# Optimization experiments

Measured on AMD Instinct MI355X. Metric: run time of the kernel, lower is better.

The kernel has to match this reference:

```python
import jax, jax.numpy as jnp
import numpy as np

IN_F = 128
OUT_F = 64
HEAD = 4
ALPHA = 0.1
N, S = 32, 1024
OH = OUT_F * HEAD


def setup_inputs() -> dict:
    key = jax.random.key(0)
    k_h, k_adj, k_W, k_a = jax.random.split(key, 4)
    h = jax.random.normal(k_h, (N, S, IN_F), dtype=jnp.float32)
    adj = jax.random.uniform(k_adj, (N, S, S), dtype=jnp.float32)
    # xavier_uniform with gain=1.414
    gain = 1.414
    lim_W = gain * np.sqrt(6.0 / (IN_F + OH))
    W = jax.random.uniform(k_W, (IN_F, OH), dtype=jnp.float32, minval=-lim_W, maxval=lim_W)
    lim_a = gain * np.sqrt(6.0 / (2 * OH + 1))
    a = jax.random.uniform(k_a, (2 * OH, 1), dtype=jnp.float32, minval=-lim_a, maxval=lim_a)
    return {"h": h, "adj": adj, "W": W, "a": a}


def reference(h, adj, W, a):
    # h: (N, S, F_in); adj unused in original forward
    Wh = jnp.einsum('nsf,fo->nso', h, W)  # (N, S, OH)
    a1 = a[:OH, 0]   # source half of concat weight
    a2 = a[OH:, 0]   # target half
    # concat([Wh_i, Wh_j]) @ a == Wh_i@a1 + Wh_j@a2  (avoids (N,S,S,2*OH) tensor)
    f = Wh @ a1  # (N, S)
    g = Wh @ a2  # (N, S)
    e = f[:, :, None] + g[:, None, :]          # (N, S, S)
    e = jnp.where(e > 0, e, ALPHA * e)          # LeakyReLU
    attention = jax.nn.softmax(e, axis=2)
    out = jnp.einsum('nij,njo->nio', attention, Wh)  # (N, S, OH)
    # split into HEAD chunks of OUT_F, stack, mean over heads
    out = out.reshape(N, S, HEAD, OUT_F).mean(axis=2)
    # ELU
    return jnp.where(out > 0, out, jnp.expm1(out))
```

## Files before the change

### kernel.cpp

```cpp
#include <hip/hip_runtime.h>
#include <math.h>

#define SQ    1024
#define INF   128
#define OUTF  64
#define OHH   256
#define LOG2E 1.44269504088896f

using bf16x8 = __attribute__((ext_vector_type(8))) __bf16;
using bf16x4 = __attribute__((ext_vector_type(4))) __bf16;
using f32x4  = __attribute__((ext_vector_type(4))) float;
using u16x8  = __attribute__((ext_vector_type(8))) unsigned short;

#if __has_builtin(__builtin_amdgcn_exp2f)
#define EXP2F(x) __builtin_amdgcn_exp2f(x)
#else
#define EXP2F(x) __expf((x) * 0.6931471805599453f)
#endif

__global__ __launch_bounds__(256) void kA(
    const float* __restrict__ h, const float* __restrict__ W,
    const float* __restrict__ a, __bf16* __restrict__ whmH,
    __bf16* __restrict__ whmL, float* __restrict__ fo, float* __restrict__ go)
{
    __shared__ __bf16 wmfH[8192];
    __shared__ __bf16 wmfL[8192];
    __shared__ float  wfl[INF], wgl[INF];
    __shared__ float  al[2 * OHH];

    const int t    = threadIdx.x;
    const int lane = t & 63;
    const int w    = t >> 6;
    const int R0   = blockIdx.x * 64;

    al[t]       = a[t];
    al[t + 256] = a[t + 256];

    for (int g = t; g < 2048; g += 256) {
        const int k  = g >> 4;
        const int n0 = (g & 15) << 2;
        const float* Wp = W + k * OHH + n0;
        float4 w0 = *(const float4*)Wp;
        float4 w1 = *(const float4*)(Wp + 64);
        float4 w2 = *(const float4*)(Wp + 128);
        float4 w3 = *(const float4*)(Wp + 192);
        float wm4[4] = {0.25f * (w0.x + w1.x + w2.x + w3.x),
                        0.25f * (w0.y + w1.y + w2.y + w3.y),
                        0.25f * (w0.z + w1.z + w2.z + w3.z),
                        0.25f * (w0.w + w1.w + w2.w + w3.w)};
        const int c = k >> 5, kq = (k >> 3) & 3, id8 = k & 7, T = n0 >> 4;
        const int lbase = kq * 16 + (n0 & 15);
        #pragma unroll
        for (int j = 0; j < 4; ++j) {
            float  v  = wm4[j];
            __bf16 hb = (__bf16)v;
            const int o = ((c * 4 + T) * 64 + lbase + j) * 8 + id8;
            wmfH[o] = hb;
            wmfL[o] = (__bf16)(v - (float)hb);
        }
    }
    __syncthreads();

    {
        const int row = t & 127;
        const float4* Wr = (const float4*)(W + row * OHH);
        const float4* av = (const float4*)(t < 128 ? al : al + OHH);
        float s = 0.f;
        for (int q = 0; q < OHH / 4; ++q) {
            float4 wv = Wr[q], x = av[q];
            s += wv.x * x.x + wv.y * x.y + wv.z * x.z + wv.w * x.w;
        }
        if (t < 128) wfl[row] = s * LOG2E;
        else         wgl[row] = s * LOG2E;
    }
    __syncthreads();

    const int m  = lane & 15;
    const int kq = lane >> 4;
    const float* hrow = h + (size_t)(R0 + w * 16 + m) * INF + kq * 8;

    f32x4 acc[4] = {};
    float sf = 0.f, sg = 0.f;

    #pragma unroll
    for (int c = 0; c < 4; ++c) {
        float4 v0 = *(const float4*)(hrow + c * 32);
        float4 v1 = *(const float4*)(hrow + c * 32 + 4);
        float hv[8] = {v0.x, v0.y, v0.z, v0.w, v1.x, v1.y, v1.z, v1.w};

        float4 wf0 = *(const float4*)(wfl + c * 32 + kq * 8);
        float4 wf1 = *(const float4*)(wfl + c * 32 + kq * 8 + 4);
        float4 wg0 = *(const float4*)(wgl + c * 32 + kq * 8);
        float4 wg1 = *(const float4*)(wgl + c * 32 + kq * 8 + 4);
        float wfv[8] = {wf0.x, wf0.y, wf0.z, wf0.w, wf1.x, wf1.y, wf1.z, wf1.w};
        float wgv[8] = {wg0.x, wg0.y, wg0.z, wg0.w, wg1.x, wg1.y, wg1.z, wg1.w};

        u16x8  ahu;
        bf16x8 alo;
        #pragma unroll
        for (int i = 0; i < 8; ++i) {
            float v = hv[i];
            sf = fmaf(v, wfv[i], sf);
            sg = fmaf(v, wgv[i], sg);
            unsigned u = __float_as_uint(v);
            ahu[i] = (unsigned short)(u >> 16);
            alo[i] = (__bf16)(v - __uint_as_float(u & 0xFFFF0000u));
        }
        bf16x8 ah = __builtin_bit_cast(bf16x8, ahu);

        #pragma unroll
        for (int T = 0; T < 4; ++T) {
            bf16x8 bh = *(const bf16x8*)&wmfH[((c * 4 + T) * 64 + lane) * 8];
            bf16x8 bl = *(const bf16x8*)&wmfL[((c * 4 + T) * 64 + lane) * 8];
            acc[T] = __builtin_amdgcn_mfma_f32_16x16x32_bf16(ah,  bh, acc[T], 0, 0, 0);
            acc[T] = __builtin_amdgcn_mfma_f32_16x16x32_bf16(alo, bh, acc[T], 0, 0, 0);
            acc[T] = __builtin_amdgcn_mfma_f32_16x16x32_bf16(ah,  bl, acc[T], 0, 0, 0);
        }
    }

    sf += __shfl_xor(sf, 16, 64); sf += __shfl_xor(sf, 32, 64);
    sg += __shfl_xor(sg, 16, 64); sg += __shfl_xor(sg, 32, 64);
    if (lane < 16) {
        fo[R0 + w * 16 + m] = sf;
        go[R0 + w * 16 + m] = sg;
    }

    {
        const int n     = R0 >> 10;
        const int Jb    = ((R0 & 1023) >> 5) + (w >> 1);
        const int jj3   = 2 * (w & 1) + (kq >> 1);
        const int laneS = jj3 * 16 + m;
        const int idx0  = (kq & 1) * 4;
        #pragma unroll
        for (int T = 0; T < 4; ++T) {
            const size_t base =
                (((size_t)(n * 32 + Jb) * 4 + T) * 64 + laneS) * 8 + idx0;
            bf16x4 hv, lv;
            #pragma unroll
            for (int r = 0; r < 4; ++r) {
                float  v  = acc[T][r];
                __bf16 hb = (__bf16)v;
                hv[r] = hb;
                lv[r] = (__bf16)(v - (float)hb);
            }
            *(bf16x4*)(whmH + base) = hv;
            *(bf16x4*)(whmL + base) = lv;
        }
    }
}

__global__ __launch_bounds__(256) void kC(
    const __bf16* __restrict__ whmH, const __bf16* __restrict__ whmL,
    const float* __restrict__ fi, const float* __restrict__ gi,
    float* __restrict__ out)
{
    __shared__ float  gl[SQ];
    __shared__ float  fl[64];
    __shared__ __bf16 bfr[3][4096];

    const int t     = threadIdx.x;
    const int lane  = t & 63;
    const int wid   = t >> 6;
    const int n     = blockIdx.x & 31;
    const int itile = blockIdx.x >> 5;
    const int i0    = itile * 64;

    const char* gHb = (const char*)(whmH + (size_t)n * 65536) + wid * 1024 + lane * 16;
    const char* gLb = (const char*)(whmL + (size_t)n * 65536) + wid * 1024 + lane * 16;

    auto stage = [&](int J, int buf) {
        char* lH = (char*)&bfr[buf][0] + wid * 1024;
        char* lL = (char*)&bfr[buf][2048] + wid * 1024;
        __builtin_amdgcn_global_load_lds(
            (const __attribute__((address_space(1))) unsigned int*)(gHb + (size_t)J * 4096),
            (__attribute__((address_space(3))) unsigned int*)lH, 16, 0, 0);
        __builtin_amdgcn_global_load_lds(
            (const __attribute__((address_space(1))) unsigned int*)(gLb + (size_t)J * 4096),
            (__attribute__((address_space(3))) unsigned int*)lL, 16, 0, 0);
    };

    ((float4*)gl)[t] = ((const float4*)(gi + n * SQ))[t];
    if (t < 64) fl[t] = fi[n * SQ + i0 + t];

    stage(0, 0);
    stage(1, 1);
    __syncthreads();

    const float myf = fl[wid * 16 + (lane & 15)];
    const int   kq  = lane >> 4;

    f32x4 acc[4] = {};
    float lsum = 0.f;

    for (int J = 0; J < 32; ++J) {
        float4 g0 = *(const float4*)&gl[J * 32 + kq * 8];
        float4 g1 = *(const float4*)&gl[J * 32 + kq * 8 + 4];
        float gs8[8] = {g0.x, g0.y, g0.z, g0.w, g1.x, g1.y, g1.z, g1.w};

        u16x8  phu;
        bf16x8 pl;
        #pragma unroll
        for (int idx = 0; idx < 8; ++idx) {
            float e  = myf + gs8[idx];
            float lr = fmaxf(e, 0.1f * e);
            float p  = EXP2F(lr);
            lsum += p;
            unsigned u = __float_as_uint(p);
            phu[idx] = (unsigned short)(u >> 16);
            pl[idx]  = (__bf16)(p - __uint_as_float(u & 0xFFFF0000u));
        }
        bf16x8 ph = __builtin_bit_cast(bf16x8, phu);

        __syncthreads();
        if (J + 2 < 32) stage(J + 2, (J + 2) % 3);

        const bf16x8* fr = (const bf16x8*)&bfr[J % 3][0];
        #pragma unroll
        for (int T = 0; T < 4; ++T) {
            bf16x8 bh = fr[T * 64 + lane];
            bf16x8 bl = fr[(4 + T) * 64 + lane];
            acc[T] = __builtin_amdgcn_mfma_f32_16x16x32_bf16(ph, bh, acc[T], 0, 0, 0);
            acc[T] = __builtin_amdgcn_mfma_f32_16x16x32_bf16(pl, bh, acc[T], 0, 0, 0);
            acc[T] = __builtin_amdgcn_mfma_f32_16x16x32_bf16(ph, bl, acc[T], 0, 0, 0);
        }
    }

    lsum += __shfl_xor(lsum, 16, 64);
    lsum += __shfl_xor(lsum, 32, 64);
    const float rv = 1.0f / lsum;

    const int rq = lane >> 4;
    float scs[4];
    #pragma unroll
    for (int r = 0; r < 4; ++r)
        scs[r] = __shfl(rv, rq * 4 + r, 64);

    const int colbase = lane & 15;
    #pragma unroll
    for (int T = 0; T < 4; ++T) {
        #pragma unroll
        for (int r = 0; r < 4; ++r) {
            int   rr = rq * 4 + r;
            float v  = acc[T][r] * scs[r];
            v = v > 0.f ? v : expm1f(v);
            out[(size_t)(n * SQ + i0 + wid * 16 + rr) * OUTF + T * 16 + colbase] = v;
        }
    }
}

extern "C" void kernel_launch(void* const* d_in, const int* in_sizes, int n_in,
                              void* d_out, int out_size, void* d_ws, size_t ws_size,
                              hipStream_t stream) {
    const float* h = (const float*)d_in[0];
    const float* W = (const float*)d_in[2];
    const float* a = (const float*)d_in[3];

    char* ws = (char*)d_ws;
    __bf16* whmH = (__bf16*)ws;
    __bf16* whmL = (__bf16*)(ws + (size_t)4 * 1024 * 1024);
    float*  fb   = (float*)(ws + (size_t)8 * 1024 * 1024);
    float*  gb   = (float*)(ws + (size_t)8 * 1024 * 1024 + 131072);
    float*  outp = (float*)d_out;

    hipLaunchKernelGGL(kA, dim3(512), dim3(256), 0, stream, h, W, a, whmH, whmL, fb, gb);
    hipLaunchKernelGGL(kC, dim3(512), dim3(256), 0, stream, whmH, whmL, fb, gb, outp);
}
```

Baseline: 215.6 us.

## Split J range across wave pairs, load B fragments directly into registers

kC is reorganised so each wave computes 32 rows (two 16-row tiles) over half of the J range. It reuses each B fragment for two MFMA row tiles and reads B straight from global memory into registers with software double-buffering, replacing the LDS triple-buffered staging and the per-iteration barriers. Partial accumulators and row sums are combined across wave pairs through LDS at the end, and launch bounds request two blocks per CU. kA's block-to-row mapping is also permuted. The cost is higher register pressure and an extra LDS reduction, plus B loads that are no longer shared via LDS.

```diff
diff --git a/kernel.cpp b/kernel.cpp
--- a/kernel.cpp
+++ b/kernel.cpp
@@ -31,7 +31,8 @@
     const int t    = threadIdx.x;
     const int lane = t & 63;
     const int w    = t >> 6;
-    const int R0   = blockIdx.x * 64;
+    const int bx   = blockIdx.x;
+    const int R0   = ((bx & 31) << 10) + ((bx >> 5) << 6);
 
     al[t]       = a[t];
     al[t + 256] = a[t + 256];
@@ -149,101 +150,125 @@
     }
 }
 
-__global__ __launch_bounds__(256) void kC(
+__global__ __launch_bounds__(256, 2) void kC(
     const __bf16* __restrict__ whmH, const __bf16* __restrict__ whmL,
     const float* __restrict__ fi, const float* __restrict__ gi,
     float* __restrict__ out)
 {
-    __shared__ float  gl[SQ];
-    __shared__ float  fl[64];
-    __shared__ __bf16 bfr[3][4096];
+    __shared__ float gl[SQ];
+    __shared__ float fl[64];
+    __shared__ f32x4 accX[4][4][64];
+    __shared__ float lsW[4][2][16];
 
     const int t     = threadIdx.x;
     const int lane  = t & 63;
     const int wid   = t >> 6;
+    const int p     = wid >> 1;
+    const int jh    = wid & 1;
     const int n     = blockIdx.x & 31;
     const int itile = blockIdx.x >> 5;
     const int i0    = itile * 64;
 
-    const char* gHb = (const char*)(whmH + (size_t)n * 65536) + wid * 1024 + lane * 16;
-    const char* gLb = (const char*)(whmL + (size_t)n * 65536) + wid * 1024 + lane * 16;
-
-    auto stage = [&](int J, int buf) {
-        char* lH = (char*)&bfr[buf][0] + wid * 1024;
-        char* lL = (char*)&bfr[buf][2048] + wid * 1024;
-        __builtin_amdgcn_global_load_lds(
-            (const __attribute__((address_space(1))) unsigned int*)(gHb + (size_t)J * 4096),
-            (__attribute__((address_space(3))) unsigned int*)lH, 16, 0, 0);
-        __builtin_amdgcn_global_load_lds(
-            (const __attribute__((address_space(1))) unsigned int*)(gLb + (size_t)J * 4096),
-            (__attribute__((address_space(3))) unsigned int*)lL, 16, 0, 0);
-    };
-
     ((float4*)gl)[t] = ((const float4*)(gi + n * SQ))[t];
     if (t < 64) fl[t] = fi[n * SQ + i0 + t];
-
-    stage(0, 0);
-    stage(1, 1);
-    __syncthreads();
-
-    const float myf = fl[wid * 16 + (lane & 15)];
-    const int   kq  = lane >> 4;
-
-    f32x4 acc[4] = {};
-    float lsum = 0.f;
-
-    for (int J = 0; J < 32; ++J) {
+    __syncthreads();
+
+    const int m  = lane & 15;
+    const int kq = lane >> 4;
+    const float myf0 = fl[p * 32 + m];
+    const float myf1 = fl[p * 32 + 16 + m];
+
+    const bf16x8* BH = (const bf16x8*)whmH + (size_t)n * 8192 + lane;
+    const bf16x8* BL = (const bf16x8*)whmL + (size_t)n * 8192 + lane;
+
+    f32x4 acc[2][4] = {};
+    float ls0 = 0.f, ls1 = 0.f;
+    const int J0 = jh * 16;
+
+    auto loadB = [&](int J, bf16x8* bh, bf16x8* bl) {
+        const bf16x8* ph_ = BH + (size_t)J * 256;
+        const bf16x8* pl_ = BL + (size_t)J * 256;
+        #pragma unroll
+        for (int T = 0; T < 4; ++T) { bh[T] = ph_[T * 64]; bl[T] = pl_[T * 64]; }
+    };
+
+    auto compute = [&](int J, const bf16x8* bh, const bf16x8* bl) {
         float4 g0 = *(const float4*)&gl[J * 32 + kq * 8];
         float4 g1 = *(const float4*)&gl[J * 32 + kq * 8 + 4];
         float gs8[8] = {g0.x, g0.y, g0.z, g0.w, g1.x, g1.y, g1.z, g1.w};
 
-        u16x8  phu;
-        bf16x8 pl;
+        u16x8  phu0, phu1;
+        bf16x8 pl0, pl1;
         #pragma unroll
         for (int idx = 0; idx < 8; ++idx) {
-            float e  = myf + gs8[idx];
-            float lr = fmaxf(e, 0.1f * e);
-            float p  = EXP2F(lr);
-            lsum += p;
-            unsigned u = __float_as_uint(p);
-            phu[idx] = (unsigned short)(u >> 16);
-            pl[idx]  = (__bf16)(p - __uint_as_float(u & 0xFFFF0000u));
-        }
-        bf16x8 ph = __builtin_bit_cast(bf16x8, phu);
-
-        __syncthreads();
-        if (J + 2 < 32) stage(J + 2, (J + 2) % 3);
-
-        const bf16x8* fr = (const bf16x8*)&bfr[J % 3][0];
+            float e0 = myf0 + gs8[idx];
+            float r0 = fmaxf(e0, 0.1f * e0);
+            float p0 = EXP2F(r0);
+            ls0 += p0;
+            unsigned u0 = __float_as_uint(p0);
+            phu0[idx] = (unsigned short)(u0 >> 16);
+            pl0[idx]  = (__bf16)(p0 - __uint_as_float(u0 & 0xFFFF0000u));
+
+            float e1 = myf1 + gs8[idx];
+            float r1 = fmaxf(e1, 0.1f * e1);
+            float p1 = EXP2F(r1);
+            ls1 += p1;
+            unsigned u1 = __float_as_uint(p1);
+            phu1[idx] = (unsigned short)(u1 >> 16);
+            pl1[idx]  = (__bf16)(p1 - __uint_as_float(u1 & 0xFFFF0000u));
+        }
+        bf16x8 ph0 = __builtin_bit_cast(bf16x8, phu0);
+        bf16x8 ph1 = __builtin_bit_cast(bf16x8, phu1);
+
         #pragma unroll
         for (int T = 0; T < 4; ++T) {
-            bf16x8 bh = fr[T * 64 + lane];
-            bf16x8 bl = fr[(4 + T) * 64 + lane];
-            acc[T] = __builtin_amdgcn_mfma_f32_16x16x32_bf16(ph, bh, acc[T], 0, 0, 0);
-            acc[T] = __builtin_amdgcn_mfma_f32_16x16x32_bf16(pl, bh, acc[T], 0, 0, 0);
-            acc[T] = __builtin_amdgcn_mfma_f32_16x16x32_bf16(ph, bl, acc[T], 0, 0, 0);
-        }
-    }
-
-    lsum += __shfl_xor(lsum, 16, 64);
-    lsum += __shfl_xor(lsum, 32, 64);
-    const float rv = 1.0f / lsum;
+            acc[0][T] = __builtin_amdgcn_mfma_f32_16x16x32_bf16(ph0, bh[T], acc[0][T], 0, 0, 0);
+            acc[0][T] = __builtin_amdgcn_mfma_f32_16x16x32_bf16(pl0, bh[T], acc[0][T], 0, 0, 0);
+            acc[0][T] = __builtin_amdgcn_mfma_f32_16x16x32_bf16(ph0, bl[T], acc[0][T], 0, 0, 0);
+            acc[1][T] = __builtin_amdgcn_mfma_f32_16x16x32_bf16(ph1, bh[T], acc[1][T], 0, 0, 0);
+            acc[1][T] = __builtin_amdgcn_mfma_f32_16x16x32_bf16(pl1, bh[T], acc[1][T], 0, 0, 0);
+            acc[1][T] = __builtin_amdgcn_mfma_f32_16x16x32_bf16(ph1, bl[T], acc[1][T], 0, 0, 0);
+        }
+    };
+
+    bf16x8 bhA[4], blA[4], bhB[4], blB[4];
+    loadB(J0, bhA, blA);
+    #pragma unroll 1
+    for (int Jt = 0; Jt < 16; Jt += 2) {
+        loadB(J0 + Jt + 1, bhB, blB);
+        compute(J0 + Jt, bhA, blA);
+        if (Jt + 2 < 16) loadB(J0 + Jt + 2, bhA, blA);
+        compute(J0 + Jt + 1, bhB, blB);
+    }
+
+    ls0 += __shfl_xor(ls0, 16, 64); ls0 += __shfl_xor(ls0, 32, 64);
+    ls1 += __shfl_xor(ls1, 16, 64); ls1 += __shfl_xor(ls1, 32, 64);
+    if (lane < 16) { lsW[wid][0][lane] = ls0; lsW[wid][1][lane] = ls1; }
+
+    #pragma unroll
+    for (int T = 0; T < 4; ++T)
+        accX[wid][T][lane] = jh ? acc[0][T] : acc[1][T];
+    __syncthreads();
 
     const int rq = lane >> 4;
-    float scs[4];
-    #pragma unroll
-    for (int r = 0; r < 4; ++r)
-        scs[r] = __shfl(rv, rq * 4 + r, 64);
-
+    float rvv[4];
+    #pragma unroll
+    for (int r = 0; r < 4; ++r) {
+        int row = rq * 4 + r;
+        rvv[r] = 1.0f / (lsW[2 * p][jh][row] + lsW[2 * p + 1][jh][row]);
+    }
     const int colbase = lane & 15;
+    const int orow0   = i0 + p * 32 + jh * 16;
     #pragma unroll
     for (int T = 0; T < 4; ++T) {
+        f32x4 mine = jh ? acc[1][T] : acc[0][T];
+        f32x4 oth  = accX[wid ^ 1][T][lane];
         #pragma unroll
         for (int r = 0; r < 4; ++r) {
             int   rr = rq * 4 + r;
-            float v  = acc[T][r] * scs[r];
+            float v  = (mine[r] + oth[r]) * rvv[r];
             v = v > 0.f ? v : expm1f(v);
-            out[(size_t)(n * SQ + i0 + wid * 16 + rr) * OUTF + T * 16 + colbase] = v;
+            out[(size_t)(n * SQ + orow0 + rr) * OUTF + T * 16 + colbase] = v;
         }
     }
 }
```

Result: slower. 222.7 us (+3.3%).

## Replace dense attention matmul with sorted prefix/suffix sums over LeakyReLU split

Applied to the files above, without the earlier changes.

Because the scores are rank-1 (f_i + g_j) and LeakyReLU is piecewise linear, each row's softmax-weighted sum splits into the j with g_j > -f_i, weighted by exp(f)exp(g), and the rest, weighted by exp(0.1f)exp(0.1g). A new kernel sorts g per batch with a bitonic sort, then builds exponentially weighted prefix and suffix sums of Wh rows and weights. The final kernel binary-searches each f_i and combines two precomputed rows. This replaces the O(S^2) MFMA pass with O(S log S) work, but the sort/scan kernel runs on only 32 blocks, and the unnormalised exp2 sums risk overflow or precision loss.

```diff
diff --git a/kernel.cpp b/kernel.cpp
--- a/kernel.cpp
+++ b/kernel.cpp
@@ -5,10 +5,10 @@
 #define INF   128
 #define OUTF  64
 #define OHH   256
+#define TSTR  66
 #define LOG2E 1.44269504088896f
 
 using bf16x8 = __attribute__((ext_vector_type(8))) __bf16;
-using bf16x4 = __attribute__((ext_vector_type(4))) __bf16;
 using f32x4  = __attribute__((ext_vector_type(4))) float;
 using u16x8  = __attribute__((ext_vector_type(8))) unsigned short;
 
@@ -20,8 +20,8 @@
 
 __global__ __launch_bounds__(256) void kA(
     const float* __restrict__ h, const float* __restrict__ W,
-    const float* __restrict__ a, __bf16* __restrict__ whmH,
-    __bf16* __restrict__ whmL, float* __restrict__ fo, float* __restrict__ go)
+    const float* __restrict__ a, float* __restrict__ whm,
+    float* __restrict__ fo, float* __restrict__ go)
 {
     __shared__ __bf16 wmfH[8192];
     __shared__ __bf16 wmfL[8192];
@@ -31,7 +31,8 @@
     const int t    = threadIdx.x;
     const int lane = t & 63;
     const int w    = t >> 6;
-    const int R0   = blockIdx.x * 64;
+    const int bx   = blockIdx.x;
+    const int R0   = ((bx & 31) << 10) + ((bx >> 5) << 6);
 
     al[t]       = a[t];
     al[t + 256] = a[t + 256];
@@ -125,126 +126,231 @@
         go[R0 + w * 16 + m] = sg;
     }
 
-    {
-        const int n     = R0 >> 10;
-        const int Jb    = ((R0 & 1023) >> 5) + (w >> 1);
-        const int jj3   = 2 * (w & 1) + (kq >> 1);
-        const int laneS = jj3 * 16 + m;
-        const int idx0  = (kq & 1) * 4;
-        #pragma unroll
-        for (int T = 0; T < 4; ++T) {
-            const size_t base =
-                (((size_t)(n * 32 + Jb) * 4 + T) * 64 + laneS) * 8 + idx0;
-            bf16x4 hv, lv;
-            #pragma unroll
-            for (int r = 0; r < 4; ++r) {
-                float  v  = acc[T][r];
-                __bf16 hb = (__bf16)v;
-                hv[r] = hb;
-                lv[r] = (__bf16)(v - (float)hb);
-            }
-            *(bf16x4*)(whmH + base) = hv;
-            *(bf16x4*)(whmL + base) = lv;
-        }
-    }
-}
-
-__global__ __launch_bounds__(256) void kC(
-    const __bf16* __restrict__ whmH, const __bf16* __restrict__ whmL,
-    const float* __restrict__ fi, const float* __restrict__ gi,
-    float* __restrict__ out)
-{
-    __shared__ float  gl[SQ];
-    __shared__ float  fl[64];
-    __shared__ __bf16 bfr[3][4096];
-
-    const int t     = threadIdx.x;
-    const int lane  = t & 63;
-    const int wid   = t >> 6;
-    const int n     = blockIdx.x & 31;
-    const int itile = blockIdx.x >> 5;
-    const int i0    = itile * 64;
-
-    const char* gHb = (const char*)(whmH + (size_t)n * 65536) + wid * 1024 + lane * 16;
-    const char* gLb = (const char*)(whmL + (size_t)n * 65536) + wid * 1024 + lane * 16;
-
-    auto stage = [&](int J, int buf) {
-        char* lH = (char*)&bfr[buf][0] + wid * 1024;
-        char* lL = (char*)&bfr[buf][2048] + wid * 1024;
-        __builtin_amdgcn_global_load_lds(
-            (const __attribute__((address_space(1))) unsigned int*)(gHb + (size_t)J * 4096),
-            (__attribute__((address_space(3))) unsigned int*)lH, 16, 0, 0);
-        __builtin_amdgcn_global_load_lds(
-            (const __attribute__((address_space(1))) unsigned int*)(gLb + (size_t)J * 4096),
-            (__attribute__((address_space(3))) unsigned int*)lL, 16, 0, 0);
-    };
-
-    ((float4*)gl)[t] = ((const float4*)(gi + n * SQ))[t];
-    if (t < 64) fl[t] = fi[n * SQ + i0 + t];
-
-    stage(0, 0);
-    stage(1, 1);
-    __syncthreads();
-
-    const float myf = fl[wid * 16 + (lane & 15)];
-    const int   kq  = lane >> 4;
-
-    f32x4 acc[4] = {};
-    float lsum = 0.f;
-
-    for (int J = 0; J < 32; ++J) {
-        float4 g0 = *(const float4*)&gl[J * 32 + kq * 8];
-        float4 g1 = *(const float4*)&gl[J * 32 + kq * 8 + 4];
-        float gs8[8] = {g0.x, g0.y, g0.z, g0.w, g1.x, g1.y, g1.z, g1.w};
-
-        u16x8  phu;
-        bf16x8 pl;
-        #pragma unroll
-        for (int idx = 0; idx < 8; ++idx) {
-            float e  = myf + gs8[idx];
-            float lr = fmaxf(e, 0.1f * e);
-            float p  = EXP2F(lr);
-            lsum += p;
-            unsigned u = __float_as_uint(p);
-            phu[idx] = (unsigned short)(u >> 16);
-            pl[idx]  = (__bf16)(p - __uint_as_float(u & 0xFFFF0000u));
-        }
-        bf16x8 ph = __builtin_bit_cast(bf16x8, phu);
-
-        __syncthreads();
-        if (J + 2 < 32) stage(J + 2, (J + 2) % 3);
-
-        const bf16x8* fr = (const bf16x8*)&bfr[J % 3][0];
-        #pragma unroll
-        for (int T = 0; T < 4; ++T) {
-            bf16x8 bh = fr[T * 64 + lane];
-            bf16x8 bl = fr[(4 + T) * 64 + lane];
-            acc[T] = __builtin_amdgcn_mfma_f32_16x16x32_bf16(ph, bh, acc[T], 0, 0, 0);
-            acc[T] = __builtin_amdgcn_mfma_f32_16x16x32_bf16(pl, bh, acc[T], 0, 0, 0);
-            acc[T] = __builtin_amdgcn_mfma_f32_16x16x32_bf16(ph, bl, acc[T], 0, 0, 0);
-        }
-    }
-
-    lsum += __shfl_xor(lsum, 16, 64);
-    lsum += __shfl_xor(lsum, 32, 64);
-    const float rv = 1.0f / lsum;
-
-    const int rq = lane >> 4;
-    float scs[4];
-    #pragma unroll
-    for (int r = 0; r < 4; ++r)
-        scs[r] = __shfl(rv, rq * 4 + r, 64);
-
-    const int colbase = lane & 15;
     #pragma unroll
     for (int T = 0; T < 4; ++T) {
         #pragma unroll
         for (int r = 0; r < 4; ++r) {
-            int   rr = rq * 4 + r;
-            float v  = acc[T][r] * scs[r];
-            v = v > 0.f ? v : expm1f(v);
-            out[(size_t)(n * SQ + i0 + wid * 16 + rr) * OUTF + T * 16 + colbase] = v;
-        }
+            whm[(size_t)(R0 + w * 16 + kq * 4 + r) * OUTF + T * 16 + m] = acc[T][r];
+        }
+    }
+}
+
+__global__ __launch_bounds__(256) void kB(
+    const float* __restrict__ whm, const float* __restrict__ gi,
+    float* __restrict__ gs_out, float* __restrict__ sufA,
+    float* __restrict__ preB)
+{
+    __shared__ unsigned long long keys[1024];
+    __shared__ unsigned short     piL[1024];
+    __shared__ float              wSuf[1024];
+    __shared__ float              wPre[1024];
+    __shared__ float              totals[2][16][TSTR];
+
+    const int t    = threadIdx.x;
+    const int lane = t & 63;
+    const int wid  = t >> 6;
+    const int n    = blockIdx.x;
+
+    for (int i = t; i < 1024; i += 256) {
+        unsigned u   = __float_as_uint(gi[n * SQ + i]);
+        unsigned key = (u & 0x80000000u) ? ~u : (u | 0x80000000u);
+        keys[i] = ((unsigned long long)key << 32) | (unsigned)i;
+    }
+    __syncthreads();
+
+    for (int k = 2; k <= 1024; k <<= 1) {
+        for (int j = k >> 1; j > 0; j >>= 1) {
+            for (int i = t; i < 1024; i += 256) {
+                int p = i ^ j;
+                if (p > i) {
+                    unsigned long long av = keys[i], bv = keys[p];
+                    bool asc = ((i & k) == 0);
+                    if ((av > bv) == asc) { keys[i] = bv; keys[p] = av; }
+                }
+            }
+            __syncthreads();
+        }
+    }
+
+    for (int i = t; i < 1024; i += 256) {
+        unsigned long long kk = keys[i];
+        unsigned key = (unsigned)(kk >> 32);
+        unsigned u   = (key & 0x80000000u) ? (key & 0x7fffffffu) : ~key;
+        float g = __uint_as_float(u);
+        piL[i]  = (unsigned short)(kk & 1023u);
+        wSuf[i] = EXP2F(g);
+        wPre[i] = EXP2F(0.1f * g);
+        gs_out[n * SQ + i] = g;
+    }
+    __syncthreads();
+
+    const float* wb = whm + (size_t)n * (SQ * OUTF);
+
+    for (int s = 0; s < 8; ++s) {
+        const int un  = s * 4 + wid;
+        const int dir = un >> 4;
+        const int c   = un & 15;
+        float acc = 0.f, dacc = 0.f;
+        if (dir == 0) {
+            float* Gp = preB + ((size_t)n * 1025 + (size_t)c * 64) * TSTR;
+            for (int q0 = 0; q0 < 64; q0 += 16) {
+                float vals[16], wv[16];
+                #pragma unroll
+                for (int u = 0; u < 16; ++u) {
+                    int tt = c * 64 + q0 + u;
+                    wv[u]   = wPre[tt];
+                    vals[u] = wb[(size_t)piL[tt] * OUTF + lane];
+                }
+                #pragma unroll
+                for (int u = 0; u < 16; ++u) {
+                    float* row = Gp + (size_t)(q0 + u) * TSTR;
+                    row[lane] = acc;
+                    if (lane == 0) row[64] = dacc;
+                    acc  = fmaf(wv[u], vals[u], acc);
+                    dacc += wv[u];
+                }
+            }
+            totals[0][c][lane] = acc;
+            if (lane == 0) totals[0][c][64] = dacc;
+        } else {
+            float* Gs = sufA + ((size_t)n * 1025 + (size_t)c * 64) * TSTR;
+            for (int q0 = 48; q0 >= 0; q0 -= 16) {
+                float vals[16], wv[16];
+                #pragma unroll
+                for (int u = 0; u < 16; ++u) {
+                    int tt = c * 64 + q0 + u;
+                    wv[u]   = wSuf[tt];
+                    vals[u] = wb[(size_t)piL[tt] * OUTF + lane];
+                }
+                #pragma unroll
+                for (int u = 15; u >= 0; --u) {
+                    acc  = fmaf(wv[u], vals[u], acc);
+                    dacc += wv[u];
+                    float* row = Gs + (size_t)(q0 + u) * TSTR;
+                    row[lane] = acc;
+                    if (lane == 0) row[64] = dacc;
+                }
+            }
+            totals[1][c][lane] = acc;
+            if (lane == 0) totals[1][c][64] = dacc;
+        }
+    }
+    __syncthreads();
+
+    for (int s = 0; s < 8; ++s) {
+        const int un  = s * 4 + wid;
+        const int dir = un >> 4;
+        const int c   = un & 15;
+        if (dir == 0) {
+            float base = 0.f, based = 0.f;
+            for (int cc = 0; cc < c; ++cc) {
+                base  += totals[0][cc][lane];
+                based += totals[0][cc][64];
+            }
+            float* Gp = preB + ((size_t)n * 1025 + (size_t)c * 64) * TSTR;
+            if (c > 0) {
+                for (int q0 = 0; q0 < 64; q0 += 16) {
+                    float vv[16], vd[16];
+                    #pragma unroll
+                    for (int u = 0; u < 16; ++u) {
+                        float* row = Gp + (size_t)(q0 + u) * TSTR;
+                        vv[u] = row[lane];
+                        vd[u] = row[64];
+                    }
+                    #pragma unroll
+                    for (int u = 0; u < 16; ++u) {
+                        float* row = Gp + (size_t)(q0 + u) * TSTR;
+                        row[lane] = vv[u] + base;
+                        if (lane == 0) row[64] = vd[u] + based;
+                    }
+                }
+            }
+            if (c == 15) {
+                float* row = preB + ((size_t)n * 1025 + 1024) * TSTR;
+                row[lane] = base + totals[0][15][lane];
+                if (lane == 0) row[64] = based + totals[0][15][64];
+            }
+        } else {
+            float base = 0.f, based = 0.f;
+            for (int cc = c + 1; cc < 16; ++cc) {
+                base  += totals[1][cc][lane];
+                based += totals[1][cc][64];
+            }
+            float* Gs = sufA + ((size_t)n * 1025 + (size_t)c * 64) * TSTR;
+            if (c < 15) {
+                for (int q0 = 0; q0 < 64; q0 += 16) {
+                    float vv[16], vd[16];
+                    #pragma unroll
+                    for (int u = 0; u < 16; ++u) {
+                        float* row = Gs + (size_t)(q0 + u) * TSTR;
+                        vv[u] = row[lane];
+                        vd[u] = row[64];
+                    }
+                    #pragma unroll
+                    for (int u = 0; u < 16; ++u) {
+                        float* row = Gs + (size_t)(q0 + u) * TSTR;
+                        row[lane] = vv[u] + base;
+                        if (lane == 0) row[64] = vd[u] + based;
+                    }
+                }
+            } else {
+                float* row = sufA + ((size_t)n * 1025 + 1024) * TSTR;
+                row[lane] = 0.f;
+                if (lane == 0) row[64] = 0.f;
+            }
+        }
+    }
+}
+
+__global__ __launch_bounds__(256) void kD(
+    const float* __restrict__ fi, const float* __restrict__ gs,
+    const float* __restrict__ sufA, const float* __restrict__ preB,
+    float* __restrict__ out)
+{
+    __shared__ float gsL[1025];
+
+    const int t    = threadIdx.x;
+    const int lane = t & 63;
+    const int wid  = t >> 6;
+    const int n    = blockIdx.x & 31;
+    const int i0   = (blockIdx.x >> 5) * 64;
+
+    for (int q = t; q < 1024; q += 256) gsL[q] = gs[n * SQ + q];
+    if (t == 0) gsL[1024] = 3.0e38f;
+    __syncthreads();
+
+    const float myf = fi[n * SQ + i0 + wid * 16 + (lane & 15)];
+    {
+    }
+    const float v = -myf;
+    int lo = 0, hi = 1024;
+    #pragma unroll
+    for (int it = 0; it < 10; ++it) {
+        int mid = (lo + hi) >> 1;
+        bool gt = gsL[mid] > v;
+        hi = gt ? mid : hi;
+        lo = gt ? lo : mid + 1;
+    }
+
+    const float* SA = sufA + (size_t)n * 1025 * TSTR;
+    const float* PB = preB + (size_t)n * 1025 * TSTR;
+    const size_t orow0 = (size_t)(n * SQ + i0 + wid * 16);
+
+    #pragma unroll 4
+    for (int s = 0; s < 16; ++s) {
+        int   r  = __shfl(lo,  s, 64);
+        float fv = __shfl(myf, s, 64);
+        const float* sa = SA + (size_t)r * TSTR;
+        const float* pb = PB + (size_t)r * TSTR;
+        float sv = sa[lane], pv = pb[lane];
+        float sd = sa[64],  pd = pb[64];
+        float eP = EXP2F(fv);
+        float eN = EXP2F(0.1f * fv);
+        float num = eP * sv + eN * pv;
+        float den = eP * sd + eN * pd;
+        float o = num / den;
+        o = o > 0.f ? o : expm1f(o);
+        out[(orow0 + s) * OUTF + lane] = o;
     }
 }
 
@@ -256,12 +362,16 @@
     const float* a = (const float*)d_in[3];
 
     char* ws = (char*)d_ws;
-    __bf16* whmH = (__bf16*)ws;
-    __bf16* whmL = (__bf16*)(ws + (size_t)4 * 1024 * 1024);
-    float*  fb   = (float*)(ws + (size_t)8 * 1024 * 1024);
-    float*  gb   = (float*)(ws + (size_t)8 * 1024 * 1024 + 131072);
-    float*  outp = (float*)d_out;
-
-    hipLaunchKernelGGL(kA, dim3(512), dim3(256), 0, stream, h, W, a, whmH, whmL, fb, gb);
-    hipLaunchKernelGGL(kC, dim3(512), dim3(256), 0, stream, whmH, whmL, fb, gb, outp);
+    const size_t MB = 1024 * 1024;
+    float* whm  = (float*)(ws);
+    float* fb   = (float*)(ws + 8 * MB);
+    float* gb   = (float*)(ws + 8 * MB + 131072);
+    float* gsO  = (float*)(ws + 8 * MB + 262144);
+    float* sufA = (float*)(ws + 9 * MB);
+    float* preB = (float*)(ws + 18 * MB);
+    float* outp = (float*)d_out;
+
+    hipLaunchKernelGGL(kA, dim3(512), dim3(256), 0, stream, h, W, a, whm, fb, gb);
+    hipLaunchKernelGGL(kB, dim3(32),  dim3(256), 0, stream, whm, gb, gsO, sufA, preB);
+    hipLaunchKernelGGL(kD, dim3(512), dim3(256), 0, stream, fb, gsO, sufA, preB, outp);
 }
```

New measurement: 303.6 us. +40.8%, slower.
